# Performance work log

Hardware: AMD Instinct MI355X
Metric: run time of the kernel (lower is better)

Reference implementation:

```python
import jax, jax.numpy as jnp
import numpy as np

B, D, H, S = 65536, 256, 4, 64
HD = D // H  # head_dim = 64
EPS = 1e-8


def _lin(x, W, b):
    # torch nn.Linear: y = x @ W.T + b, W: [out, in]
    return x @ W.T + b


def _cos_attn(q_heads, keys, vals):
    # q_heads: [B,H,hd]; keys/vals: [H,S,hd] (shared across batch)
    qn = q_heads / (jnp.linalg.norm(q_heads, axis=-1, keepdims=True) + EPS)
    kn = keys / (jnp.linalg.norm(keys, axis=-1, keepdims=True) + EPS)
    sim = jnp.einsum('bhd,hsd->bhs', qn, kn)          # cosine sims, temp=1.0
    attn = jax.nn.softmax(sim, axis=-1)
    return jnp.einsum('bhs,hsd->bhd', attn, vals)     # [B,H,hd]


def setup_inputs() -> dict:
    key = jax.random.key(0)
    ks = jax.random.split(key, 20)

    def xavier(k, shape):
        fan_in, fan_out = shape[1], shape[0]
        lim = np.sqrt(6.0 / (fan_in + fan_out))
        return jax.random.uniform(k, shape, jnp.float32, -lim, lim)

    return {
        'query': jax.random.normal(ks[0], (B, D), jnp.float32),
        'context': jax.random.normal(ks[1], (B, D), jnp.float32),
        'fast_keys': 0.01 * jax.random.normal(ks[2], (H, S, HD), jnp.float32),
        'fast_vals': 0.01 * jax.random.normal(ks[3], (H, S, HD), jnp.float32),
        'deep_keys': 0.01 * jax.random.normal(ks[4], (H, S, HD), jnp.float32),
        'deep_vals': 0.01 * jax.random.normal(ks[5], (H, S, HD), jnp.float32),
        'Wq': xavier(ks[6], (D, D)), 'bq': jnp.zeros((D,), jnp.float32),
        'Wg': xavier(ks[7], (D, D)), 'bg': jnp.zeros((D,), jnp.float32),
        'Wc1': xavier(ks[8], (D // 2, D)), 'bc1': jnp.zeros((D // 2,), jnp.float32),
        'Wc2': xavier(ks[9], (1, D // 2)), 'bc2': jnp.zeros((1,), jnp.float32),
        'Wo': xavier(ks[10], (D, D)), 'bo': jnp.zeros((D,), jnp.float32),
        'Ws': xavier(ks[11], (D, D)), 'bs': jnp.zeros((D,), jnp.float32),
        'mix_logit': jnp.zeros((), jnp.float32),
        'surprise_mean': jnp.zeros((1, D), jnp.float32),
        'surprise_var': jnp.ones((1, D), jnp.float32),
    }


def reference(query, context, fast_keys, fast_vals, deep_keys, deep_vals,
              Wq, bq, Wg, bg, Wc1, bc1, Wc2, bc2, Wo, bo, Ws, bs,
              mix_logit, surprise_mean, surprise_var):
    # --- query projection and head split ---
    q = _lin(query, Wq, bq)                       # [B, D]
    q_heads = q.reshape(B, H, HD)                 # [B, H, hd]

    # --- dual-tier cosine-similarity attention reads ---
    v_fast = _cos_attn(q_heads, fast_keys, fast_vals).reshape(B, D)
    v_deep = _cos_attn(q_heads, deep_keys, deep_vals).reshape(B, D)

    # --- context-gated mixing of tiers ---
    gate = jnp.tanh(_lin(context, Wg, bg)).mean(axis=-1, keepdims=True)  # [B,1]
    mix = jax.nn.sigmoid(mix_logit + gate)
    out = mix * v_fast + (1.0 - mix) * v_deep

    # --- adaptive retrieval confidence head ---
    conf = jax.nn.sigmoid(_lin(jnp.tanh(_lin(context, Wc1, bc1)), Wc2, bc2))  # [B,1]
    out = out * conf
    out = _lin(out, Wo, bo)                       # [B, d_value]

    # --- surprise (detached diagnostic, does not feed output) ---
    h = jax.lax.stop_gradient(_lin(context, Ws, bs))
    z = (h - surprise_mean) / jnp.sqrt(surprise_var + 1e-6)
    surprise = jax.nn.sigmoid(jnp.abs(z).mean(axis=-1) - 2.0)  # 1/max(0.5,0.1)=2.0
    del surprise  # aux diagnostic; main output is the retrieved vector
    return out
```

## Files before the change

kernel.cpp:

```cpp
#include <hip/hip_runtime.h>

typedef unsigned short u16;
typedef __attribute__((ext_vector_type(8))) short bf16x8;
typedef __attribute__((ext_vector_type(4))) float f32x4;
typedef __attribute__((ext_vector_type(4))) unsigned short u16x4;
typedef __attribute__((ext_vector_type(8))) unsigned short u16x8;

#define MFMA16(a, b, c) __builtin_amdgcn_mfma_f32_16x16x32_bf16((a), (b), (c), 0, 0, 0)

#define OFF_WQ   0
#define OFF_WG   65536
#define OFF_WC1  131072
#define OFF_WO   163840
#define OFF_KNF  229376
#define OFF_VTF  245760
#define OFF_KND  262144
#define OFF_VTD  278528

__device__ __forceinline__ u16 f2b(float f) {
  union { float f; unsigned u; } v; v.f = f;
  unsigned r = v.u + 0x7fffu + ((v.u >> 16) & 1u);
  return (u16)(r >> 16);
}
__device__ __forceinline__ unsigned pk2(float lo, float hi) {
  unsigned r;
  asm("v_cvt_pk_bf16_f32 %0, %1, %2" : "=v"(r) : "v"(lo), "v"(hi));
  return r;
}
__device__ __forceinline__ float fsig(float x) {
  return __builtin_amdgcn_rcpf(1.f + __expf(-x));
}
__device__ __forceinline__ float ftanh(float x) {
  float e = __expf(2.f * x);
  return (e - 1.f) * __builtin_amdgcn_rcpf(e + 1.f);
}
__device__ __forceinline__ float sum16(float v) {
  v += __shfl_xor(v, 1);
  v += __shfl_xor(v, 2);
  v += __shfl_xor(v, 4);
  v += __shfl_xor(v, 8);
  return v;
}

__global__ void k_prep(const float* __restrict__ Wq, const float* __restrict__ Wg,
                       const float* __restrict__ Wc1, const float* __restrict__ Wo,
                       const float* __restrict__ fk, const float* __restrict__ fv,
                       const float* __restrict__ dk, const float* __restrict__ dv,
                       u16* __restrict__ ws) {
  const int bid = blockIdx.x, t = threadIdx.x;
  if (bid < 96) {
    const float* W = bid < 32 ? Wq : (bid < 64 ? Wg : Wo);
    const int OFF = bid < 32 ? OFF_WQ : (bid < 64 ? OFF_WG : OFF_WO);
    int c = (bid & 31) * 256 + t;
    int lane = c & 63, nt = (c >> 6) & 1, kk = (c >> 7) & 7, w = c >> 10;
    const float* s = W + (w * 32 + nt * 16 + (lane & 15)) * 256 + kk * 32 + ((lane >> 4) & 3) * 8;
    u16x8 o;
    #pragma unroll
    for (int j = 0; j < 8; ++j) o[j] = f2b(s[j]);
    *(u16x8*)(ws + OFF + c * 8) = o;
  } else if (bid < 112) {
    int c = (bid - 96) * 256 + t;
    int lane = c & 63, kk = (c >> 6) & 7, w = c >> 9;
    const float* s = Wc1 + (w * 16 + (lane & 15)) * 256 + kk * 32 + ((lane >> 4) & 3) * 8;
    u16x8 o;
    #pragma unroll
    for (int j = 0; j < 8; ++j) o[j] = f2b(s[j]);
    *(u16x8*)(ws + OFF_WC1 + c * 8) = o;
  } else {
    int idx = (bid - 112) * 256 + t;
    int st = idx >> 8, rowid = idx & 255;
    int h = rowid >> 6, s = rowid & 63;
    if (st < 2) {
      const float* p = (st == 0 ? fk : dk) + rowid * 64;
      const int OFF = (st == 0) ? OFF_KNF : OFF_KND;
      float ss = 0.f;
      #pragma unroll
      for (int d = 0; d < 64; ++d) { float x = p[d]; ss += x * x; }
      float sc = __builtin_amdgcn_rcpf(__builtin_amdgcn_sqrtf(ss) + 1e-8f);
      int nt = s >> 4, sl = s & 15;
      #pragma unroll
      for (int d = 0; d < 64; ++d) {
        int lane = ((d >> 3) & 3) * 16 + sl;
        ws[OFF + (((h * 2 + (d >> 5)) * 4 + nt) * 64 + lane) * 8 + (d & 7)] = f2b(p[d] * sc);
      }
    } else {
      const float* p = (st == 2 ? fv : dv) + rowid * 64;
      const int OFF = (st == 2) ? OFF_VTF : OFF_VTD;
      int kk = s >> 5, quad = (s >> 3) & 3, j = s & 7;
      #pragma unroll
      for (int d = 0; d < 64; ++d) {
        int lane = quad * 16 + (d & 15);
        ws[OFF + (((h * 2 + kk) * 4 + (d >> 4)) * 64 + lane) * 8 + j] = f2b(p[d]);
      }
    }
  }
}

__global__ __launch_bounds__(512, 4)
void k_fused(const float* __restrict__ query, const float* __restrict__ context,
             const float* __restrict__ bq, const float* __restrict__ bg,
             const float* __restrict__ bc1, const float* __restrict__ Wc2,
             const float* __restrict__ bc2v, const float* __restrict__ bo,
             const float* __restrict__ mixl, const u16* __restrict__ ws,
             float* __restrict__ outp) {
  __shared__ u16 sX[64 * 256];
  __shared__ u16 sY[64 * 256];
  __shared__ float red_a[8][64];
  __shared__ float red_c[8][64];
  __shared__ float red_q[8][64];
  __shared__ float sA[64];
  __shared__ float sB[64];

  const int t = threadIdx.x;
  const int w = t >> 6;
  const int lane = t & 63;
  const int quad = lane >> 4;
  const int l16 = lane & 15;
  const int row4 = quad * 4;
  const int h = w >> 1;
  const int rh = (w & 1) * 32;
  const int blk = blockIdx.x;
  char* Xb = (char*)sX;
  char* Yb = (char*)sY;
  char* Ch = Xb + h * 8192;

  auto stage = [&](char* dstB, const float* src) {
    #pragma unroll
    for (int i = 0; i < 8; ++i) {
      int e = i * 2048 + t * 4;
      float4 v = *(const float4*)(src + e);
      int row = e >> 8, col = e & 255;
      uint2 pk;
      pk.x = pk2(v.x, v.y);
      pk.y = pk2(v.z, v.w);
      *(uint2*)(dstB + row * 512 + ((((col >> 3) ^ (row & 7)) << 4) | ((col & 7) << 1))) = pk;
    }
  };
  auto ldA = [&](const char* B, int row, int kb) {
    return *(const bf16x8*)(B + row * 512 + ((((kb >> 3) ^ (row & 7)) << 4)));
  };
  auto ldC = [&](int row, int kb) {
    return *(const bf16x8*)(Ch + row * 128 + ((((kb >> 3) ^ (row & 7)) << 4)));
  };
  auto cwr = [&](int row, int col, u16 v) {
    *(u16*)(Ch + row * 128 + (((((col >> 3) ^ (row & 7)) << 3) | (col & 7)) << 1)) = v;
  };
  auto ywr = [&](int row, int col, u16 v) {
    *(u16*)(Yb + row * 512 + (((((col >> 3) ^ (row & 7)) << 3) | (col & 7)) << 1)) = v;
  };

  const f32x4 vzero = {0.f, 0.f, 0.f, 0.f};

  stage(Xb, context + (size_t)blk * 16384);
  stage(Yb, query + (size_t)blk * 16384);
  float bgv[2], bqv[2], bov[2];
  #pragma unroll
  for (int nt = 0; nt < 2; ++nt) {
    int n = w * 32 + nt * 16 + l16;
    bgv[nt] = bg[n]; bqv[nt] = bq[n]; bov[nt] = bo[n];
  }
  float bc1v = bc1[w * 16 + l16];
  float wc2v = Wc2[w * 16 + l16];
  __syncthreads();

  {
    f32x4 ag[4][2], ac[4];
    #pragma unroll
    for (int mt = 0; mt < 4; ++mt) { ag[mt][0] = vzero; ag[mt][1] = vzero; ac[mt] = vzero; }
    #pragma unroll
    for (int kk = 0; kk < 8; ++kk) {
      int kb = kk * 32 + quad * 8;
      bf16x8 a0 = ldA(Xb, l16, kb), a1 = ldA(Xb, 16 + l16, kb),
             a2 = ldA(Xb, 32 + l16, kb), a3 = ldA(Xb, 48 + l16, kb);
      #pragma unroll
      for (int nt = 0; nt < 2; ++nt) {
        bf16x8 b = *(const bf16x8*)(ws + OFF_WG + (((w * 8 + kk) * 2 + nt) * 64 + lane) * 8);
        ag[0][nt] = MFMA16(a0, b, ag[0][nt]);
        ag[1][nt] = MFMA16(a1, b, ag[1][nt]);
        ag[2][nt] = MFMA16(a2, b, ag[2][nt]);
        ag[3][nt] = MFMA16(a3, b, ag[3][nt]);
      }
      bf16x8 bc = *(const bf16x8*)(ws + OFF_WC1 + ((w * 8 + kk) * 64 + lane) * 8);
      ac[0] = MFMA16(a0, bc, ac[0]);
      ac[1] = MFMA16(a1, bc, ac[1]);
      ac[2] = MFMA16(a2, bc, ac[2]);
      ac[3] = MFMA16(a3, bc, ac[3]);
    }
    #pragma unroll
    for (int mt = 0; mt < 4; ++mt)
      #pragma unroll
      for (int r = 0; r < 4; ++r) {
        float sg = ftanh(ag[mt][0][r] + bgv[0]) + ftanh(ag[mt][1][r] + bgv[1]);
        sg = sum16(sg);
        float sc = ftanh(ac[mt][r] + bc1v) * wc2v;
        sc = sum16(sc);
        if (l16 == 0) { red_a[w][mt * 16 + row4 + r] = sg; red_c[w][mt * 16 + row4 + r] = sc; }
      }
  }
  __syncthreads();

  if (t < 64) {
    float g = 0.f, cc = 0.f;
    #pragma unroll
    for (int i = 0; i < 8; ++i) { g += red_a[i][t]; cc += red_c[i][t]; }
    float mix = fsig(mixl[0] + g * (1.f / 256.f));
    float conf = fsig(cc + bc2v[0]);
    sA[t] = conf * mix;
    sB[t] = conf - conf * mix;
  }
  f32x4 qa[4][2];
  {
    #pragma unroll
    for (int mt = 0; mt < 4; ++mt) { qa[mt][0] = vzero; qa[mt][1] = vzero; }
    #pragma unroll
    for (int kk = 0; kk < 8; ++kk) {
      int kb = kk * 32 + quad * 8;
      bf16x8 a0 = ldA(Yb, l16, kb), a1 = ldA(Yb, 16 + l16, kb),
             a2 = ldA(Yb, 32 + l16, kb), a3 = ldA(Yb, 48 + l16, kb);
      #pragma unroll
      for (int nt = 0; nt < 2; ++nt) {
        bf16x8 b = *(const bf16x8*)(ws + OFF_WQ + (((w * 8 + kk) * 2 + nt) * 64 + lane) * 8);
        qa[0][nt] = MFMA16(a0, b, qa[0][nt]);
        qa[1][nt] = MFMA16(a1, b, qa[1][nt]);
        qa[2][nt] = MFMA16(a2, b, qa[2][nt]);
        qa[3][nt] = MFMA16(a3, b, qa[3][nt]);
      }
    }
    #pragma unroll
    for (int mt = 0; mt < 4; ++mt)
      #pragma unroll
      for (int r = 0; r < 4; ++r) {
        float ss = 0.f;
        #pragma unroll
        for (int nt = 0; nt < 2; ++nt) {
          float q_ = qa[mt][nt][r] + bqv[nt];
          qa[mt][nt][r] = q_;
          ss += q_ * q_;
        }
        ss = sum16(ss);
        if (l16 == 0) red_q[w][mt * 16 + row4 + r] = ss;
      }
  }
  __syncthreads();

  #pragma unroll
  for (int mt = 0; mt < 4; ++mt)
    #pragma unroll
    for (int r = 0; r < 4; ++r) {
      int row = mt * 16 + row4 + r;
      float ss = red_q[w][row] + red_q[w ^ 1][row];
      float scl = __builtin_amdgcn_rcpf(__builtin_amdgcn_sqrtf(ss) + 1e-8f);
      #pragma unroll
      for (int nt = 0; nt < 2; ++nt)
        cwr(row, (w & 1) * 32 + nt * 16 + l16, f2b(qa[mt][nt][r] * scl));
    }
  __syncthreads();

  #pragma unroll
  for (int half = 0; half < 2; ++half) {
    const int r0 = rh + half * 16;
    bf16x8 q0 = ldC(r0 + l16, quad * 8);
    bf16x8 q1 = ldC(r0 + l16, 32 + quad * 8);
    f32x4 oa[4];

    #pragma unroll
    for (int tier = 0; tier < 2; ++tier) {
      const u16* KN = ws + (tier == 0 ? OFF_KNF : OFF_KND);
      const u16* VT = ws + (tier == 0 ? OFF_VTF : OFF_VTD);

      f32x4 s4[4];
      #pragma unroll
      for (int nt = 0; nt < 4; ++nt) s4[nt] = vzero;
      #pragma unroll
      for (int kk = 0; kk < 2; ++kk)
        #pragma unroll
        for (int nt = 0; nt < 4; ++nt) {
          bf16x8 b = *(const bf16x8*)(KN + (((h * 2 + kk) * 4 + nt) * 64 + lane) * 8);
          s4[nt] = MFMA16(kk ? q1 : q0, b, s4[nt]);
        }

      #pragma unroll
      for (int r = 0; r < 4; ++r) {
        float rs = 0.f;
        #pragma unroll
        for (int nt = 0; nt < 4; ++nt) { float e = __expf(s4[nt][r]); s4[nt][r] = e; rs += e; }
        rs = sum16(rs);
        float inv = __builtin_amdgcn_rcpf(rs);
        int row = r0 + row4 + r;
        #pragma unroll
        for (int nt = 0; nt < 4; ++nt) cwr(row, nt * 16 + l16, f2b(s4[nt][r] * inv));
      }

      bf16x8 p0 = ldC(r0 + l16, quad * 8);
      bf16x8 p1 = ldC(r0 + l16, 32 + quad * 8);
      f32x4 pv4[4];
      #pragma unroll
      for (int nt = 0; nt < 4; ++nt) pv4[nt] = vzero;
      #pragma unroll
      for (int kk = 0; kk < 2; ++kk)
        #pragma unroll
        for (int nt = 0; nt < 4; ++nt) {
          bf16x8 b = *(const bf16x8*)(VT + (((h * 2 + kk) * 4 + nt) * 64 + lane) * 8);
          pv4[nt] = MFMA16(kk ? p1 : p0, b, pv4[nt]);
        }

      #pragma unroll
      for (int r = 0; r < 4; ++r) {
        int row = r0 + row4 + r;
        float m_ = (tier == 0) ? sA[row] : sB[row];
        #pragma unroll
        for (int nt = 0; nt < 4; ++nt) {
          if (tier == 0) oa[nt][r] = m_ * pv4[nt][r];
          else           oa[nt][r] += m_ * pv4[nt][r];
        }
      }
    }

    #pragma unroll
    for (int r = 0; r < 4; ++r) {
      int row = r0 + row4 + r;
      #pragma unroll
      for (int nt = 0; nt < 4; ++nt)
        ywr(row, h * 64 + nt * 16 + l16, f2b(oa[nt][r]));
    }
  }
  __syncthreads();

  {
    f32x4 o[4][2];
    #pragma unroll
    for (int mt = 0; mt < 4; ++mt) { o[mt][0] = vzero; o[mt][1] = vzero; }
    #pragma unroll
    for (int kk = 0; kk < 8; ++kk) {
      int kb = kk * 32 + quad * 8;
      bf16x8 a0 = ldA(Yb, l16, kb), a1 = ldA(Yb, 16 + l16, kb),
             a2 = ldA(Yb, 32 + l16, kb), a3 = ldA(Yb, 48 + l16, kb);
      #pragma unroll
      for (int nt = 0; nt < 2; ++nt) {
        bf16x8 b = *(const bf16x8*)(ws + OFF_WO + (((w * 8 + kk) * 2 + nt) * 64 + lane) * 8);
        o[0][nt] = MFMA16(a0, b, o[0][nt]);
        o[1][nt] = MFMA16(a1, b, o[1][nt]);
        o[2][nt] = MFMA16(a2, b, o[2][nt]);
        o[3][nt] = MFMA16(a3, b, o[3][nt]);
      }
    }
    float* dst = outp + (size_t)blk * 16384;
    #pragma unroll
    for (int mt = 0; mt < 4; ++mt)
      #pragma unroll
      for (int r = 0; r < 4; ++r) {
        int row = mt * 16 + row4 + r;
        #pragma unroll
        for (int nt = 0; nt < 2; ++nt)
          dst[row * 256 + w * 32 + nt * 16 + l16] = o[mt][nt][r] + bov[nt];
      }
  }
}

extern "C" void kernel_launch(void* const* d_in, const int* in_sizes, int n_in,
                              void* d_out, int out_size, void* d_ws, size_t ws_size,
                              hipStream_t stream) {
  const float* query   = (const float*)d_in[0];
  const float* context = (const float*)d_in[1];
  const float* fk      = (const float*)d_in[2];
  const float* fv      = (const float*)d_in[3];
  const float* dk      = (const float*)d_in[4];
  const float* dv      = (const float*)d_in[5];
  const float* Wq      = (const float*)d_in[6];
  const float* bq      = (const float*)d_in[7];
  const float* Wg      = (const float*)d_in[8];
  const float* bg      = (const float*)d_in[9];
  const float* Wc1     = (const float*)d_in[10];
  const float* bc1     = (const float*)d_in[11];
  const float* Wc2     = (const float*)d_in[12];
  const float* bc2     = (const float*)d_in[13];
  const float* Wo      = (const float*)d_in[14];
  const float* bo      = (const float*)d_in[15];
  const float* mixl    = (const float*)d_in[18];
  u16* ws = (u16*)d_ws;
  float* outp = (float*)d_out;

  k_prep<<<116, 256, 0, stream>>>(Wq, Wg, Wc1, Wo, fk, fv, dk, dv, ws);
  k_fused<<<1024, 512, 0, stream>>>(query, context, bq, bg, bc1, Wc2, bc2, bo,
                                    mixl, ws, outp);
}
```

Before: 281.3 us.

## Remap query projection so each wave owns a full head; prefetch weights

The Q projection is repartitioned so each wave computes a full 64-wide head for 32 rows. This lets the query L2 norm run inside one wave and removes the red_q shared reduction and one block barrier. Softmax and output stores now pack two bf16 values per shuffle-assisted 32-bit LDS write instead of scalar u16 writes. The first weight fragments for each GEMM are also prefetched ahead of barriers. The prep kernel is rewritten so one wave handles each key/value row using shuffle reductions, with more blocks launched. The cost is extra shuffles and register pressure.

```diff
diff --git a/kernel.cpp b/kernel.cpp
--- a/kernel.cpp
+++ b/kernel.cpp
@@ -3,7 +3,6 @@
 typedef unsigned short u16;
 typedef __attribute__((ext_vector_type(8))) short bf16x8;
 typedef __attribute__((ext_vector_type(4))) float f32x4;
-typedef __attribute__((ext_vector_type(4))) unsigned short u16x4;
 typedef __attribute__((ext_vector_type(8))) unsigned short u16x8;
 
 #define MFMA16(a, b, c) __builtin_amdgcn_mfma_f32_16x16x32_bf16((a), (b), (c), 0, 0, 0)
@@ -67,31 +66,26 @@
     for (int j = 0; j < 8; ++j) o[j] = f2b(s[j]);
     *(u16x8*)(ws + OFF_WC1 + c * 8) = o;
   } else {
-    int idx = (bid - 112) * 256 + t;
-    int st = idx >> 8, rowid = idx & 255;
-    int h = rowid >> 6, s = rowid & 63;
+    int unit = (bid - 112) * 4 + (t >> 6);
+    int lane = t & 63;
+    int st = unit >> 8, rowid = unit & 255;
+    int hh = rowid >> 6, s = rowid & 63;
     if (st < 2) {
       const float* p = (st == 0 ? fk : dk) + rowid * 64;
-      const int OFF = (st == 0) ? OFF_KNF : OFF_KND;
-      float ss = 0.f;
-      #pragma unroll
-      for (int d = 0; d < 64; ++d) { float x = p[d]; ss += x * x; }
-      float sc = __builtin_amdgcn_rcpf(__builtin_amdgcn_sqrtf(ss) + 1e-8f);
-      int nt = s >> 4, sl = s & 15;
-      #pragma unroll
-      for (int d = 0; d < 64; ++d) {
-        int lane = ((d >> 3) & 3) * 16 + sl;
-        ws[OFF + (((h * 2 + (d >> 5)) * 4 + nt) * 64 + lane) * 8 + (d & 7)] = f2b(p[d] * sc);
-      }
+      float x = p[lane];
+      float v = x * x;
+      v += __shfl_xor(v, 1);  v += __shfl_xor(v, 2);  v += __shfl_xor(v, 4);
+      v += __shfl_xor(v, 8);  v += __shfl_xor(v, 16); v += __shfl_xor(v, 32);
+      float sc = __builtin_amdgcn_rcpf(__builtin_amdgcn_sqrtf(v) + 1e-8f);
+      int nt = s >> 4, kk = lane >> 5, lo = ((lane >> 3) & 3) * 16 + (s & 15), j = lane & 7;
+      ws[(st == 0 ? OFF_KNF : OFF_KND) + (((hh * 2 + kk) * 4 + nt) * 64 + lo) * 8 + j] =
+          f2b(x * sc);
     } else {
       const float* p = (st == 2 ? fv : dv) + rowid * 64;
-      const int OFF = (st == 2) ? OFF_VTF : OFF_VTD;
-      int kk = s >> 5, quad = (s >> 3) & 3, j = s & 7;
-      #pragma unroll
-      for (int d = 0; d < 64; ++d) {
-        int lane = quad * 16 + (d & 15);
-        ws[OFF + (((h * 2 + kk) * 4 + (d >> 4)) * 64 + lane) * 8 + j] = f2b(p[d]);
-      }
+      int kk = s >> 5, qd = (s >> 3) & 3, j = s & 7;
+      int lo = qd * 16 + (lane & 15), nt = lane >> 4;
+      ws[(st == 2 ? OFF_VTF : OFF_VTD) + (((hh * 2 + kk) * 4 + nt) * 64 + lo) * 8 + j] =
+          f2b(p[lane]);
     }
   }
 }
@@ -107,7 +101,6 @@
   __shared__ u16 sY[64 * 256];
   __shared__ float red_a[8][64];
   __shared__ float red_c[8][64];
-  __shared__ float red_q[8][64];
   __shared__ float sA[64];
   __shared__ float sB[64];
 
@@ -117,12 +110,14 @@
   const int quad = lane >> 4;
   const int l16 = lane & 15;
   const int row4 = quad * 4;
-  const int h = w >> 1;
-  const int rh = (w & 1) * 32;
+  const int l16e = l16 & ~1;
+  const int oddl = lane & 1;
+  const int hd = w & 3;
+  const int rb = (w >> 2) * 32;
   const int blk = blockIdx.x;
   char* Xb = (char*)sX;
   char* Yb = (char*)sY;
-  char* Ch = Xb + h * 8192;
+  char* Ch = Xb + w * 4096;
 
   auto stage = [&](char* dstB, const float* src) {
     #pragma unroll
@@ -139,30 +134,49 @@
   auto ldA = [&](const char* B, int row, int kb) {
     return *(const bf16x8*)(B + row * 512 + ((((kb >> 3) ^ (row & 7)) << 4)));
   };
-  auto ldC = [&](int row, int kb) {
+  auto ldCh = [&](int row, int kb) {
     return *(const bf16x8*)(Ch + row * 128 + ((((kb >> 3) ^ (row & 7)) << 4)));
   };
-  auto cwr = [&](int row, int col, u16 v) {
-    *(u16*)(Ch + row * 128 + (((((col >> 3) ^ (row & 7)) << 3) | (col & 7)) << 1)) = v;
-  };
-  auto ywr = [&](int row, int col, u16 v) {
-    *(u16*)(Yb + row * 512 + (((((col >> 3) ^ (row & 7)) << 3) | (col & 7)) << 1)) = v;
+  auto st4c = [&](int row, float v0, float v1, float v2, float v3) {
+    float o0 = __shfl_xor(v0, 1), o1 = __shfl_xor(v1, 1);
+    float o2 = __shfl_xor(v2, 1), o3 = __shfl_xor(v3, 1);
+    float lo0 = oddl ? o1 : v0, hi0 = oddl ? v1 : o0;
+    float lo1 = oddl ? o3 : v2, hi1 = oddl ? v3 : o2;
+    int c0 = (oddl ? 16 : 0) + l16e, c1 = (oddl ? 48 : 32) + l16e;
+    *(unsigned*)(Ch + row * 128 + ((((c0 >> 3) ^ (row & 7)) << 4) | ((c0 & 7) << 1))) = pk2(lo0, hi0);
+    *(unsigned*)(Ch + row * 128 + ((((c1 >> 3) ^ (row & 7)) << 4) | ((c1 & 7) << 1))) = pk2(lo1, hi1);
+  };
+  auto st4y = [&](int row, int cb, float v0, float v1, float v2, float v3) {
+    float o0 = __shfl_xor(v0, 1), o1 = __shfl_xor(v1, 1);
+    float o2 = __shfl_xor(v2, 1), o3 = __shfl_xor(v3, 1);
+    float lo0 = oddl ? o1 : v0, hi0 = oddl ? v1 : o0;
+    float lo1 = oddl ? o3 : v2, hi1 = oddl ? v3 : o2;
+    int c0 = cb + (oddl ? 16 : 0) + l16e, c1 = cb + (oddl ? 48 : 32) + l16e;
+    *(unsigned*)(Yb + row * 512 + ((((c0 >> 3) ^ (row & 7)) << 4) | ((c0 & 7) << 1))) = pk2(lo0, hi0);
+    *(unsigned*)(Yb + row * 512 + ((((c1 >> 3) ^ (row & 7)) << 4) | ((c1 & 7) << 1))) = pk2(lo1, hi1);
   };
 
   const f32x4 vzero = {0.f, 0.f, 0.f, 0.f};
+
+  bf16x8 pg0 = *(const bf16x8*)(ws + OFF_WG + ((w * 16 + 0) * 64 + lane) * 8);
+  bf16x8 pg1 = *(const bf16x8*)(ws + OFF_WG + ((w * 16 + 1) * 64 + lane) * 8);
+  bf16x8 pc0 = *(const bf16x8*)(ws + OFF_WC1 + ((w * 8) * 64 + lane) * 8);
 
   stage(Xb, context + (size_t)blk * 16384);
   stage(Yb, query + (size_t)blk * 16384);
-  float bgv[2], bqv[2], bov[2];
+  float bgv[2], bov[2], bq4[4];
   #pragma unroll
   for (int nt = 0; nt < 2; ++nt) {
     int n = w * 32 + nt * 16 + l16;
-    bgv[nt] = bg[n]; bqv[nt] = bq[n]; bov[nt] = bo[n];
-  }
+    bgv[nt] = bg[n]; bov[nt] = bo[n];
+  }
+  #pragma unroll
+  for (int nt = 0; nt < 4; ++nt) bq4[nt] = bq[hd * 64 + nt * 16 + l16];
   float bc1v = bc1[w * 16 + l16];
   float wc2v = Wc2[w * 16 + l16];
   __syncthreads();
 
+  bf16x8 pq0, pq1;
   {
     f32x4 ag[4][2], ac[4];
     #pragma unroll
@@ -172,20 +186,20 @@
       int kb = kk * 32 + quad * 8;
       bf16x8 a0 = ldA(Xb, l16, kb), a1 = ldA(Xb, 16 + l16, kb),
              a2 = ldA(Xb, 32 + l16, kb), a3 = ldA(Xb, 48 + l16, kb);
-      #pragma unroll
-      for (int nt = 0; nt < 2; ++nt) {
-        bf16x8 b = *(const bf16x8*)(ws + OFF_WG + (((w * 8 + kk) * 2 + nt) * 64 + lane) * 8);
-        ag[0][nt] = MFMA16(a0, b, ag[0][nt]);
-        ag[1][nt] = MFMA16(a1, b, ag[1][nt]);
-        ag[2][nt] = MFMA16(a2, b, ag[2][nt]);
-        ag[3][nt] = MFMA16(a3, b, ag[3][nt]);
-      }
-      bf16x8 bc = *(const bf16x8*)(ws + OFF_WC1 + ((w * 8 + kk) * 64 + lane) * 8);
+      bf16x8 b0 = kk ? *(const bf16x8*)(ws + OFF_WG + (((w * 8 + kk) * 2 + 0) * 64 + lane) * 8) : pg0;
+      bf16x8 b1 = kk ? *(const bf16x8*)(ws + OFF_WG + (((w * 8 + kk) * 2 + 1) * 64 + lane) * 8) : pg1;
+      bf16x8 bc = kk ? *(const bf16x8*)(ws + OFF_WC1 + ((w * 8 + kk) * 64 + lane) * 8) : pc0;
+      ag[0][0] = MFMA16(a0, b0, ag[0][0]); ag[0][1] = MFMA16(a0, b1, ag[0][1]);
+      ag[1][0] = MFMA16(a1, b0, ag[1][0]); ag[1][1] = MFMA16(a1, b1, ag[1][1]);
+      ag[2][0] = MFMA16(a2, b0, ag[2][0]); ag[2][1] = MFMA16(a2, b1, ag[2][1]);
+      ag[3][0] = MFMA16(a3, b0, ag[3][0]); ag[3][1] = MFMA16(a3, b1, ag[3][1]);
       ac[0] = MFMA16(a0, bc, ac[0]);
       ac[1] = MFMA16(a1, bc, ac[1]);
       ac[2] = MFMA16(a2, bc, ac[2]);
       ac[3] = MFMA16(a3, bc, ac[3]);
     }
+    pq0 = *(const bf16x8*)(ws + OFF_WQ + ((((hd * 4) >> 1) * 8 * 2 + ((hd * 4) & 1)) * 64 + lane) * 8);
+    pq1 = *(const bf16x8*)(ws + OFF_WQ + (((((hd * 4 + 1) >> 1) * 8) * 2 + ((hd * 4 + 1) & 1)) * 64 + lane) * 8);
     #pragma unroll
     for (int mt = 0; mt < 4; ++mt)
       #pragma unroll
@@ -208,10 +222,117 @@
     sA[t] = conf * mix;
     sB[t] = conf - conf * mix;
   }
-  f32x4 qa[4][2];
   {
-    #pragma unroll
-    for (int mt = 0; mt < 4; ++mt) { qa[mt][0] = vzero; qa[mt][1] = vzero; }
+    f32x4 qa[2][4];
+    #pragma unroll
+    for (int mt = 0; mt < 2; ++mt)
+      #pragma unroll
+      for (int nt = 0; nt < 4; ++nt) qa[mt][nt] = vzero;
+    #pragma unroll
+    for (int kk = 0; kk < 8; ++kk) {
+      int kb = kk * 32 + quad * 8;
+      bf16x8 a0 = ldA(Yb, rb + l16, kb), a1 = ldA(Yb, rb + 16 + l16, kb);
+      #pragma unroll
+      for (int nt = 0; nt < 4; ++nt) {
+        int g = hd * 4 + nt;
+        bf16x8 b = (kk == 0 && nt == 0) ? pq0
+                 : (kk == 0 && nt == 1) ? pq1
+                 : *(const bf16x8*)(ws + OFF_WQ + ((((g >> 1) * 8 + kk) * 2 + (g & 1)) * 64 + lane) * 8);
+        qa[0][nt] = MFMA16(a0, b, qa[0][nt]);
+        qa[1][nt] = MFMA16(a1, b, qa[1][nt]);
+      }
+    }
+    #pragma unroll
+    for (int mt = 0; mt < 2; ++mt)
+      #pragma unroll
+      for (int r = 0; r < 4; ++r) {
+        float ss = 0.f;
+        #pragma unroll
+        for (int nt = 0; nt < 4; ++nt) {
+          float q_ = qa[mt][nt][r] + bq4[nt];
+          qa[mt][nt][r] = q_;
+          ss += q_ * q_;
+        }
+        ss = sum16(ss);
+        float scl = __builtin_amdgcn_rcpf(__builtin_amdgcn_sqrtf(ss) + 1e-8f);
+        st4c(mt * 16 + row4 + r,
+             qa[mt][0][r] * scl, qa[mt][1][r] * scl, qa[mt][2][r] * scl, qa[mt][3][r] * scl);
+      }
+  }
+  __syncthreads();
+
+  #pragma unroll
+  for (int half = 0; half < 2; ++half) {
+    const int rl = half * 16;
+    bf16x8 q0 = ldCh(rl + l16, quad * 8);
+    bf16x8 q1 = ldCh(rl + l16, 32 + quad * 8);
+    f32x4 oa[4];
+
+    #pragma unroll
+    for (int tier = 0; tier < 2; ++tier) {
+      const u16* KN = ws + (tier == 0 ? OFF_KNF : OFF_KND);
+      const u16* VT = ws + (tier == 0 ? OFF_VTF : OFF_VTD);
+
+      f32x4 s4[4];
+      #pragma unroll
+      for (int nt = 0; nt < 4; ++nt) s4[nt] = vzero;
+      #pragma unroll
+      for (int kk = 0; kk < 2; ++kk)
+        #pragma unroll
+        for (int nt = 0; nt < 4; ++nt) {
+          bf16x8 b = *(const bf16x8*)(KN + (((hd * 2 + kk) * 4 + nt) * 64 + lane) * 8);
+          s4[nt] = MFMA16(kk ? q1 : q0, b, s4[nt]);
+        }
+
+      #pragma unroll
+      for (int r = 0; r < 4; ++r) {
+        float rs = 0.f;
+        #pragma unroll
+        for (int nt = 0; nt < 4; ++nt) { float e = __expf(s4[nt][r]); s4[nt][r] = e; rs += e; }
+        rs = sum16(rs);
+        float inv = __builtin_amdgcn_rcpf(rs);
+        st4c(rl + row4 + r,
+             s4[0][r] * inv, s4[1][r] * inv, s4[2][r] * inv, s4[3][r] * inv);
+      }
+
+      bf16x8 p0 = ldCh(rl + l16, quad * 8);
+      bf16x8 p1 = ldCh(rl + l16, 32 + quad * 8);
+      f32x4 pv4[4];
+      #pragma unroll
+      for (int nt = 0; nt < 4; ++nt) pv4[nt] = vzero;
+      #pragma unroll
+      for (int kk = 0; kk < 2; ++kk)
+        #pragma unroll
+        for (int nt = 0; nt < 4; ++nt) {
+          bf16x8 b = *(const bf16x8*)(VT + (((hd * 2 + kk) * 4 + nt) * 64 + lane) * 8);
+          pv4[nt] = MFMA16(kk ? p1 : p0, b, pv4[nt]);
+        }
+
+      #pragma unroll
+      for (int r = 0; r < 4; ++r) {
+        int rg = rb + rl + row4 + r;
+        float m_ = (tier == 0) ? sA[rg] : sB[rg];
+        #pragma unroll
+        for (int nt = 0; nt < 4; ++nt) {
+          if (tier == 0) oa[nt][r] = m_ * pv4[nt][r];
+          else           oa[nt][r] += m_ * pv4[nt][r];
+        }
+      }
+    }
+
+    #pragma unroll
+    for (int r = 0; r < 4; ++r)
+      st4y(rb + rl + row4 + r, hd * 64, oa[0][r], oa[1][r], oa[2][r], oa[3][r]);
+  }
+
+  bf16x8 po0 = *(const bf16x8*)(ws + OFF_WO + (((w * 8) * 2 + 0) * 64 + lane) * 8);
+  bf16x8 po1 = *(const bf16x8*)(ws + OFF_WO + (((w * 8) * 2 + 1) * 64 + lane) * 8);
+  __syncthreads();
+
+  {
+    f32x4 o[4][2];
+    #pragma unroll
+    for (int mt = 0; mt < 4; ++mt) { o[mt][0] = vzero; o[mt][1] = vzero; }
     #pragma unroll
     for (int kk = 0; kk < 8; ++kk) {
       int kb = kk * 32 + quad * 8;
@@ -219,125 +340,9 @@
              a2 = ldA(Yb, 32 + l16, kb), a3 = ldA(Yb, 48 + l16, kb);
       #pragma unroll
       for (int nt = 0; nt < 2; ++nt) {
-        bf16x8 b = *(const bf16x8*)(ws + OFF_WQ + (((w * 8 + kk) * 2 + nt) * 64 + lane) * 8);
-        qa[0][nt] = MFMA16(a0, b, qa[0][nt]);
-        qa[1][nt] = MFMA16(a1, b, qa[1][nt]);
-        qa[2][nt] = MFMA16(a2, b, qa[2][nt]);
-        qa[3][nt] = MFMA16(a3, b, qa[3][nt]);
-      }
-    }
-    #pragma unroll
-    for (int mt = 0; mt < 4; ++mt)
-      #pragma unroll
-      for (int r = 0; r < 4; ++r) {
-        float ss = 0.f;
-        #pragma unroll
-        for (int nt = 0; nt < 2; ++nt) {
-          float q_ = qa[mt][nt][r] + bqv[nt];
-          qa[mt][nt][r] = q_;
-          ss += q_ * q_;
-        }
-        ss = sum16(ss);
-        if (l16 == 0) red_q[w][mt * 16 + row4 + r] = ss;
-      }
-  }
-  __syncthreads();
-
-  #pragma unroll
-  for (int mt = 0; mt < 4; ++mt)
-    #pragma unroll
-    for (int r = 0; r < 4; ++r) {
-      int row = mt * 16 + row4 + r;
-      float ss = red_q[w][row] + red_q[w ^ 1][row];
-      float scl = __builtin_amdgcn_rcpf(__builtin_amdgcn_sqrtf(ss) + 1e-8f);
-      #pragma unroll
-      for (int nt = 0; nt < 2; ++nt)
-        cwr(row, (w & 1) * 32 + nt * 16 + l16, f2b(qa[mt][nt][r] * scl));
-    }
-  __syncthreads();
-
-  #pragma unroll
-  for (int half = 0; half < 2; ++half) {
-    const int r0 = rh + half * 16;
-    bf16x8 q0 = ldC(r0 + l16, quad * 8);
-    bf16x8 q1 = ldC(r0 + l16, 32 + quad * 8);
-    f32x4 oa[4];
-
-    #pragma unroll
-    for (int tier = 0; tier < 2; ++tier) {
-      const u16* KN = ws + (tier == 0 ? OFF_KNF : OFF_KND);
-      const u16* VT = ws + (tier == 0 ? OFF_VTF : OFF_VTD);
-
-      f32x4 s4[4];
-      #pragma unroll
-      for (int nt = 0; nt < 4; ++nt) s4[nt] = vzero;
-      #pragma unroll
-      for (int kk = 0; kk < 2; ++kk)
-        #pragma unroll
-        for (int nt = 0; nt < 4; ++nt) {
-          bf16x8 b = *(const bf16x8*)(KN + (((h * 2 + kk) * 4 + nt) * 64 + lane) * 8);
-          s4[nt] = MFMA16(kk ? q1 : q0, b, s4[nt]);
-        }
-
-      #pragma unroll
-      for (int r = 0; r < 4; ++r) {
-        float rs = 0.f;
-        #pragma unroll
-        for (int nt = 0; nt < 4; ++nt) { float e = __expf(s4[nt][r]); s4[nt][r] = e; rs += e; }
-        rs = sum16(rs);
-        float inv = __builtin_amdgcn_rcpf(rs);
-        int row = r0 + row4 + r;
-        #pragma unroll
-        for (int nt = 0; nt < 4; ++nt) cwr(row, nt * 16 + l16, f2b(s4[nt][r] * inv));
-      }
-
-      bf16x8 p0 = ldC(r0 + l16, quad * 8);
-      bf16x8 p1 = ldC(r0 + l16, 32 + quad * 8);
-      f32x4 pv4[4];
-      #pragma unroll
-      for (int nt = 0; nt < 4; ++nt) pv4[nt] = vzero;
-      #pragma unroll
-      for (int kk = 0; kk < 2; ++kk)
-        #pragma unroll
-        for (int nt = 0; nt < 4; ++nt) {
-          bf16x8 b = *(const bf16x8*)(VT + (((h * 2 + kk) * 4 + nt) * 64 + lane) * 8);
-          pv4[nt] = MFMA16(kk ? p1 : p0, b, pv4[nt]);
-        }
-
-      #pragma unroll
-      for (int r = 0; r < 4; ++r) {
-        int row = r0 + row4 + r;
-        float m_ = (tier == 0) ? sA[row] : sB[row];
-        #pragma unroll
-        for (int nt = 0; nt < 4; ++nt) {
-          if (tier == 0) oa[nt][r] = m_ * pv4[nt][r];
-          else           oa[nt][r] += m_ * pv4[nt][r];
-        }
-      }
-    }
-
-    #pragma unroll
-    for (int r = 0; r < 4; ++r) {
-      int row = r0 + row4 + r;
-      #pragma unroll
-      for (int nt = 0; nt < 4; ++nt)
-        ywr(row, h * 64 + nt * 16 + l16, f2b(oa[nt][r]));
-    }
-  }
-  __syncthreads();
-
-  {
-    f32x4 o[4][2];
-    #pragma unroll
-    for (int mt = 0; mt < 4; ++mt) { o[mt][0] = vzero; o[mt][1] = vzero; }
-    #pragma unroll
-    for (int kk = 0; kk < 8; ++kk) {
-      int kb = kk * 32 + quad * 8;
-      bf16x8 a0 = ldA(Yb, l16, kb), a1 = ldA(Yb, 16 + l16, kb),
-             a2 = ldA(Yb, 32 + l16, kb), a3 = ldA(Yb, 48 + l16, kb);
-      #pragma unroll
-      for (int nt = 0; nt < 2; ++nt) {
-        bf16x8 b = *(const bf16x8*)(ws + OFF_WO + (((w * 8 + kk) * 2 + nt) * 64 + lane) * 8);
+        bf16x8 b = (kk == 0 && nt == 0) ? po0
+                 : (kk == 0 && nt == 1) ? po1
+                 : *(const bf16x8*)(ws + OFF_WO + (((w * 8 + kk) * 2 + nt) * 64 + lane) * 8);
         o[0][nt] = MFMA16(a0, b, o[0][nt]);
         o[1][nt] = MFMA16(a1, b, o[1][nt]);
         o[2][nt] = MFMA16(a2, b, o[2][nt]);
@@ -380,7 +385,7 @@
   u16* ws = (u16*)d_ws;
   float* outp = (float*)d_out;
 
-  k_prep<<<116, 256, 0, stream>>>(Wq, Wg, Wc1, Wo, fk, fv, dk, dv, ws);
+  k_prep<<<368, 256, 0, stream>>>(Wq, Wg, Wc1, Wo, fk, fv, dk, dv, ws);
   k_fused<<<1024, 512, 0, stream>>>(query, context, bq, bg, bc1, Wc2, bc2, bo,
                                     mixl, ws, outp);
 }
```

Result: no change. 276.3 us (-1.8%).
